# Performance work log

Measured on AMD Instinct MI355X. Metric: run time of the kernel, lower is better.

Reference implementation:

```python
import jax, jax.numpy as jnp
import numpy as np

N = 100000
E = 1600000
IN_DIM, HID, OUT = 512, 128, 16


def setup_inputs() -> dict:
    key = jax.random.key(0)
    ks = jax.random.split(key, 8)
    x = jax.random.normal(ks[0], (N, IN_DIM), dtype=jnp.float32)
    edge_index = jax.random.randint(ks[1], (2, E), 0, N, dtype=jnp.int64)
    # GCNConv params (Glorot-ish scale) and Linear head
    W1 = jax.random.normal(ks[2], (IN_DIM, HID), dtype=jnp.float32) / np.sqrt(IN_DIM)
    b1 = jnp.zeros((HID,), dtype=jnp.float32)
    W2 = jax.random.normal(ks[3], (HID, HID), dtype=jnp.float32) / np.sqrt(HID)
    b2 = jnp.zeros((HID,), dtype=jnp.float32)
    Wl = jax.random.normal(ks[4], (HID, OUT), dtype=jnp.float32) / np.sqrt(HID)
    bl = jnp.zeros((OUT,), dtype=jnp.float32)
    return {"x": x, "edge_index": edge_index, "W1": W1, "b1": b1,
            "W2": W2, "b2": b2, "Wl": Wl, "bl": bl}


def _gcn_conv(x, W, b, src, dst, deg_inv_sqrt, deg_inv):
    # h = x @ W ; out[dst] += norm * h[src]; self-loop adds h[i]/deg[i]
    h = x @ W                                           # [N, D]
    norm = deg_inv_sqrt[src] * deg_inv_sqrt[dst]        # [E]
    msgs = h[src] * norm[:, None]                       # [E, D] gather
    agg = jax.ops.segment_sum(msgs, dst, num_segments=x.shape[0])  # scatter
    agg = agg + h * deg_inv[:, None]                    # self-loop term
    return agg + b


def reference(x, edge_index, W1, b1, W2, b2, Wl, bl):
    src, dst = edge_index[0], edge_index[1]
    n = x.shape[0]
    ones = jnp.ones(src.shape[0], dtype=x.dtype)
    # degree with self-loops (PyG gcn_norm counts in-degree at target + 1)
    deg = jax.ops.segment_sum(ones, dst, num_segments=n) + 1.0
    deg_inv_sqrt = jax.lax.rsqrt(deg)
    deg_inv = 1.0 / deg

    h = _gcn_conv(x, W1, b1, src, dst, deg_inv_sqrt, deg_inv)
    h = jax.nn.relu(h)
    # dropout: inference mode (training=False) -> identity
    h = _gcn_conv(h, W2, b2, src, dst, deg_inv_sqrt, deg_inv)
    embeddings = jax.nn.relu(h)
    out = embeddings @ Wl + bl
    return out, embeddings
```

## Files before the change

kernel.cpp:

```cpp
#include <hip/hip_runtime.h>

#define NN 100000
#define EE 1600000
#define IND 512
#define HIDD 128
#define OUTD 16
#define DEG_BLKS 128
#define GEMM_BLKS 1563

typedef __bf16 bf16x8 __attribute__((ext_vector_type(8)));
typedef float f32x4 __attribute__((ext_vector_type(4)));

__device__ __forceinline__ ushort f2bf(float f) {
    union { float f; uint u; } v; v.f = f;
    uint r = v.u + 0x7FFFu + ((v.u >> 16) & 1u);
    return (ushort)(r >> 16);
}

__global__ void k_prep(const float* __restrict__ W1, const float* __restrict__ W2,
                       ushort* __restrict__ Wt1, ushort* __restrict__ Wt2) {
    int b = blockIdx.x, tid = threadIdx.x;
    if (b < 256) {
        int i = b * 256 + tid;
        int k = i >> 7, n = i & 127;
        Wt1[n * 512 + k] = f2bf(W1[i]);
    } else {
        int i = (b - 256) * 256 + tid;
        int k = i >> 7, n = i & 127;
        Wt2[n * 128 + k] = f2bf(W2[i]);
    }
}

__global__ void k_scan_local(const int* __restrict__ deg, int* __restrict__ incl,
                             int* __restrict__ bsum) {
    __shared__ int s[256];
    int tid = threadIdx.x;
    int i = blockIdx.x * 256 + tid;
    int v = (i < NN) ? deg[i] : 0;
    s[tid] = v;
    __syncthreads();
    for (int off = 1; off < 256; off <<= 1) {
        int t = (tid >= off) ? s[tid - off] : 0;
        __syncthreads();
        s[tid] += t;
        __syncthreads();
    }
    if (i < NN) incl[i] = s[tid];
    if (tid == 255) bsum[blockIdx.x] = s[255];
}

__global__ void k_scan_bsum(const int* __restrict__ bsum, int* __restrict__ boff, int n) {
    __shared__ int s[512];
    int tid = threadIdx.x;
    int v = (tid < n) ? bsum[tid] : 0;
    s[tid] = v;
    __syncthreads();
    for (int off = 1; off < 512; off <<= 1) {
        int t = (tid >= off) ? s[tid - off] : 0;
        __syncthreads();
        s[tid] += t;
        __syncthreads();
    }
    if (tid < n) boff[tid] = s[tid] - v;
}

__global__ void k_scan_final(const int* __restrict__ incl, const int* __restrict__ deg,
                             const int* __restrict__ boff, int* __restrict__ rs,
                             int* __restrict__ cursor, float* __restrict__ dis,
                             float* __restrict__ dinv) {
    int i = blockIdx.x * 256 + threadIdx.x;
    if (i < NN) {
        int d = deg[i];
        int v = incl[i] + boff[i >> 8];
        int start = v - d;
        rs[i] = start;
        cursor[i] = start;
        if (i == NN - 1) rs[NN] = v;
        float df = (float)(d + 1);
        dis[i] = rsqrtf(df);
        dinv[i] = 1.0f / df;
    }
}

__global__ void k_fill(const int* __restrict__ src, const int* __restrict__ dst,
                       const float* __restrict__ dis, int* __restrict__ cursor,
                       int2* __restrict__ ew) {
    int i = blockIdx.x * blockDim.x + threadIdx.x;
    int stride = gridDim.x * blockDim.x;
    for (; i < EE; i += stride) {
        int d = dst[i];
        int s = src[i];
        int pos = atomicAdd(&cursor[d], 1);
        ew[pos] = make_int2(s, __float_as_int(dis[s] * dis[d]));
    }
}

template <int K, bool AFP32>
__device__ __forceinline__ void gemm_body(const void* __restrict__ Ap,
                                          const ushort* __restrict__ Wt,
                                          ushort* __restrict__ C, int M, int blk) {
    __shared__ ushort As[64][40];
    __shared__ ushort Ws[128][40];
    int tid = threadIdx.x;
    int row0 = blk * 64;
    int wid = tid >> 6, lane = tid & 63;
    int wm = (wid & 1) * 32, wn = (wid >> 1) * 64;
    int lm = lane & 15, lk8 = (lane >> 4) * 8;

    f32x4 acc[4][2];
#pragma unroll
    for (int q = 0; q < 4; q++)
#pragma unroll
        for (int r = 0; r < 2; r++) acc[q][r] = (f32x4){0.f, 0.f, 0.f, 0.f};

    int arow = tid >> 2, akg = tid & 3;
    int gr = row0 + arow;

    for (int k0 = 0; k0 < K; k0 += 32) {
        if (AFP32) {
            const float* A = (const float*)Ap;
            float4 v0 = make_float4(0.f, 0.f, 0.f, 0.f), v1 = v0;
            if (gr < M) {
                const float* p = A + (size_t)gr * K + k0 + akg * 8;
                v0 = *(const float4*)(p);
                v1 = *(const float4*)(p + 4);
            }
            uint4 pk;
            pk.x = (uint)f2bf(v0.x) | ((uint)f2bf(v0.y) << 16);
            pk.y = (uint)f2bf(v0.z) | ((uint)f2bf(v0.w) << 16);
            pk.z = (uint)f2bf(v1.x) | ((uint)f2bf(v1.y) << 16);
            pk.w = (uint)f2bf(v1.z) | ((uint)f2bf(v1.w) << 16);
            *(uint4*)&As[arow][akg * 8] = pk;
        } else {
            const ushort* A = (const ushort*)Ap;
            uint4 v = make_uint4(0, 0, 0, 0);
            if (gr < M) v = *(const uint4*)(A + (size_t)gr * K + k0 + akg * 8);
            *(uint4*)&As[arow][akg * 8] = v;
        }
#pragma unroll
        for (int p = 0; p < 2; p++) {
            int idx = p * 256 + tid;
            int n = idx >> 2, kg = idx & 3;
            uint4 v = *(const uint4*)(Wt + (size_t)n * K + k0 + kg * 8);
            *(uint4*)&Ws[n][kg * 8] = v;
        }
        __syncthreads();

        bf16x8 xf[2], wf[4];
#pragma unroll
        for (int r = 0; r < 2; r++) xf[r] = *(const bf16x8*)&As[wm + r * 16 + lm][lk8];
#pragma unroll
        for (int q = 0; q < 4; q++) wf[q] = *(const bf16x8*)&Ws[wn + q * 16 + lm][lk8];
#pragma unroll
        for (int q = 0; q < 4; q++)
#pragma unroll
            for (int r = 0; r < 2; r++)
                acc[q][r] = __builtin_amdgcn_mfma_f32_16x16x32_bf16(wf[q], xf[r], acc[q][r], 0, 0, 0);
        __syncthreads();
    }

    int cn4 = (lane >> 4) * 4;
#pragma unroll
    for (int r = 0; r < 2; r++) {
        int m = row0 + wm + r * 16 + lm;
        if (m < M) {
#pragma unroll
            for (int q = 0; q < 4; q++) {
                int n = wn + q * 16 + cn4;
                uint2 o;
                o.x = (uint)f2bf(acc[q][r][0]) | ((uint)f2bf(acc[q][r][1]) << 16);
                o.y = (uint)f2bf(acc[q][r][2]) | ((uint)f2bf(acc[q][r][3]) << 16);
                *(uint2*)(C + (size_t)m * 128 + n) = o;
            }
        }
    }
}

__global__ __launch_bounds__(256) void k_mega1(const float* __restrict__ x,
                                               const ushort* __restrict__ Wt1,
                                               ushort* __restrict__ C,
                                               const int* __restrict__ dst,
                                               int* __restrict__ deg) {
    if (blockIdx.x < DEG_BLKS) {
        int i = blockIdx.x * 256 + threadIdx.x;
        int stride = DEG_BLKS * 256;
        for (; i < EE; i += stride) atomicAdd(&deg[dst[i]], 1);
    } else {
        gemm_body<IND, true>(x, Wt1, C, NN, blockIdx.x - DEG_BLKS);
    }
}

__global__ __launch_bounds__(256) void k_gemm2(const ushort* __restrict__ A,
                                               const ushort* __restrict__ Wt,
                                               ushort* __restrict__ C) {
    gemm_body<HIDD, false>(A, Wt, C, NN, blockIdx.x);
}

template <bool OUTF32>
__global__ __launch_bounds__(256) void k_agg(const ushort* __restrict__ h,
                                             const int* __restrict__ rs,
                                             const int2* __restrict__ ew,
                                             const float* __restrict__ dinv,
                                             const float* __restrict__ bias,
                                             void* __restrict__ yv) {
    int node = blockIdx.x * 4 + (threadIdx.x >> 6);
    int lane = threadIdx.x & 63;
    if (node >= NN) return;
    int half = lane >> 5, c = lane & 31;
    const uint2* h64 = (const uint2*)h;

    float acc0 = 0.f, acc1 = 0.f, acc2 = 0.f, acc3 = 0.f;
    if (half == 0) {
        float dv = dinv[node];
        uint2 sv = h64[(size_t)node * 32 + c];
        acc0 = __uint_as_float(sv.x << 16) * dv;
        acc1 = __uint_as_float(sv.x & 0xffff0000u) * dv;
        acc2 = __uint_as_float(sv.y << 16) * dv;
        acc3 = __uint_as_float(sv.y & 0xffff0000u) * dv;
    }

    int e = rs[node], e1 = rs[node + 1];

#define EL(i) int2 p##i = ew[e + 2 * i + half]; \
              uint2 g##i = h64[(size_t)(uint)p##i.x * 32 + c];
#define EA(i) { float w##i = __int_as_float(p##i.y); \
    acc0 += w##i * __uint_as_float(g##i.x << 16); \
    acc1 += w##i * __uint_as_float(g##i.x & 0xffff0000u); \
    acc2 += w##i * __uint_as_float(g##i.y << 16); \
    acc3 += w##i * __uint_as_float(g##i.y & 0xffff0000u); }

    for (; e + 16 <= e1; e += 16) {
        EL(0) EL(1) EL(2) EL(3) EL(4) EL(5) EL(6) EL(7)
        EA(0) EA(1) EA(2) EA(3) EA(4) EA(5) EA(6) EA(7)
    }
    for (; e + 4 <= e1; e += 4) {
        EL(0) EL(1)
        EA(0) EA(1)
    }
    if (e + 2 <= e1) {
        EL(0)
        EA(0)
        e += 2;
    }
    if (e < e1 && half == 0) {
        int2 p = ew[e];
        uint2 g = h64[(size_t)(uint)p.x * 32 + c];
        float w = __int_as_float(p.y);
        acc0 += w * __uint_as_float(g.x << 16);
        acc1 += w * __uint_as_float(g.x & 0xffff0000u);
        acc2 += w * __uint_as_float(g.y << 16);
        acc3 += w * __uint_as_float(g.y & 0xffff0000u);
    }
#undef EL
#undef EA

    acc0 += __shfl_xor(acc0, 32, 64);
    acc1 += __shfl_xor(acc1, 32, 64);
    acc2 += __shfl_xor(acc2, 32, 64);
    acc3 += __shfl_xor(acc3, 32, 64);

    if (half == 0) {
        float4 bv = *(const float4*)(bias + c * 4);
        acc0 = fmaxf(acc0 + bv.x, 0.f);
        acc1 = fmaxf(acc1 + bv.y, 0.f);
        acc2 = fmaxf(acc2 + bv.z, 0.f);
        acc3 = fmaxf(acc3 + bv.w, 0.f);
        if (OUTF32) {
            *(float4*)((float*)yv + (size_t)node * 128 + c * 4) =
                make_float4(acc0, acc1, acc2, acc3);
        } else {
            uint2 o;
            o.x = (uint)f2bf(acc0) | ((uint)f2bf(acc1) << 16);
            o.y = (uint)f2bf(acc2) | ((uint)f2bf(acc3) << 16);
            *(uint2*)((ushort*)yv + (size_t)node * 128 + c * 4) = o;
        }
    }
}

__global__ __launch_bounds__(256) void k_out(const float* __restrict__ emb,
                                             const float* __restrict__ Wl,
                                             const float* __restrict__ bl,
                                             float* __restrict__ out) {
    __shared__ float wl_s[128 * 16];
    __shared__ float es[16][129];
    int tid = threadIdx.x;
    int row0 = blockIdx.x * 16;
#pragma unroll
    for (int p = 0; p < 8; p++) wl_s[p * 256 + tid] = Wl[p * 256 + tid];
#pragma unroll
    for (int p = 0; p < 8; p++) {
        int idx = p * 256 + tid;
        int r = idx >> 7, c = idx & 127;
        int gr = row0 + r;
        es[r][c] = (gr < NN) ? emb[(size_t)gr * 128 + c] : 0.0f;
    }
    __syncthreads();
    int r = tid >> 4, o = tid & 15;
    float acc = bl[o];
#pragma unroll
    for (int k = 0; k < 128; k++) acc += es[r][k] * wl_s[k * 16 + o];
    int gr = row0 + r;
    if (gr < NN) out[(size_t)gr * 16 + o] = acc;
}

extern "C" void kernel_launch(void* const* d_in, const int* in_sizes, int n_in,
                              void* d_out, int out_size, void* d_ws, size_t ws_size,
                              hipStream_t stream) {
    const float* x  = (const float*)d_in[0];
    const int* ei   = (const int*)d_in[1];
    const float* W1 = (const float*)d_in[2];
    const float* b1 = (const float*)d_in[3];
    const float* W2 = (const float*)d_in[4];
    const float* b2 = (const float*)d_in[5];
    const float* Wl = (const float*)d_in[6];
    const float* bl = (const float*)d_in[7];
    const int* src = ei;
    const int* dst = ei + EE;

    float* outp = (float*)d_out;
    float* emb  = outp + (size_t)NN * OUTD;

    int2* ew    = (int2*)d_ws;
    ushort* h_a = (ushort*)(ew + EE);
    ushort* h_b = h_a + (size_t)NN * 128;
    ushort* Wt1 = h_b + (size_t)NN * 128;
    ushort* Wt2 = Wt1 + 128 * 512;
    int* deg    = (int*)(Wt2 + 128 * 128);
    float* dis  = (float*)(deg + NN);
    float* dinv = dis + NN;
    int* incl   = (int*)(dinv + NN);
    int* rs     = incl + NN;
    int* cursor = rs + NN + 8;
    int* bsum   = cursor + NN;
    int* boff   = bsum + 512;

    const int NB_N = (NN + 255) / 256;

    hipMemsetAsync(deg, 0, (size_t)NN * sizeof(int), stream);
    k_prep<<<320, 256, 0, stream>>>(W1, W2, Wt1, Wt2);
    k_mega1<<<DEG_BLKS + GEMM_BLKS, 256, 0, stream>>>(x, Wt1, h_a, dst, deg);
    k_scan_local<<<NB_N, 256, 0, stream>>>(deg, incl, bsum);
    k_scan_bsum<<<1, 512, 0, stream>>>(bsum, boff, NB_N);
    k_scan_final<<<NB_N, 256, 0, stream>>>(incl, deg, boff, rs, cursor, dis, dinv);
    k_fill<<<2048, 256, 0, stream>>>(src, dst, dis, cursor, ew);

    k_agg<false><<<(NN + 3) / 4, 256, 0, stream>>>(h_a, rs, ew, dinv, b1, h_b);
    k_gemm2<<<GEMM_BLKS, 256, 0, stream>>>(h_b, Wt2, h_a);
    k_agg<true><<<(NN + 3) / 4, 256, 0, stream>>>(h_a, rs, ew, dinv, b2, emb);
    k_out<<<(NN + 15) / 16, 256, 0, stream>>>(emb, Wl, bl, outp);
}
```

Baseline: 383.0 us.

## Enlarge GEMM tile to 128 rows and prefetch next K-slice into registers

The GEMM block tile grows from 64 to 128 rows, with each warp now covering all 128 output columns, which halves the block count and the number of times the weight slice is reloaded. Global loads for the next K step are issued into registers before the MFMA work on the current step, overlapping memory latency with compute. Out-of-range rows are clamped to the last valid row instead of being zero-filled. In exchange, each thread uses more registers (16 accumulators and the prefetch buffers), which may lower occupancy, and there are now fewer blocks to cover the GPU.

```diff
diff --git a/kernel.cpp b/kernel.cpp
--- a/kernel.cpp
+++ b/kernel.cpp
@@ -6,7 +6,7 @@
 #define HIDD 128
 #define OUTD 16
 #define DEG_BLKS 128
-#define GEMM_BLKS 1563
+#define GEMM_BLKS 782
 
 typedef __bf16 bf16x8 __attribute__((ext_vector_type(8)));
 typedef float f32x4 __attribute__((ext_vector_type(4)));
@@ -99,65 +99,99 @@
 __device__ __forceinline__ void gemm_body(const void* __restrict__ Ap,
                                           const ushort* __restrict__ Wt,
                                           ushort* __restrict__ C, int M, int blk) {
-    __shared__ ushort As[64][40];
+    __shared__ ushort As[128][40];
     __shared__ ushort Ws[128][40];
     int tid = threadIdx.x;
-    int row0 = blk * 64;
+    int row0 = blk * 128;
     int wid = tid >> 6, lane = tid & 63;
-    int wm = (wid & 1) * 32, wn = (wid >> 1) * 64;
+    int wm = wid * 32;
     int lm = lane & 15, lk8 = (lane >> 4) * 8;
 
-    f32x4 acc[4][2];
-#pragma unroll
-    for (int q = 0; q < 4; q++)
+    int srow = tid >> 1;
+    int koff = (tid & 1) * 16;
+    int arow = row0 + srow;
+    if (arow >= M) arow = M - 1;
+    const float* Af = (const float*)Ap;
+    const ushort* Ab = (const ushort*)Ap;
+    const ushort* Wrow = Wt + (size_t)srow * K + koff;
+
+    f32x4 acc[8][2];
+#pragma unroll
+    for (int q = 0; q < 8; q++)
 #pragma unroll
         for (int r = 0; r < 2; r++) acc[q][r] = (f32x4){0.f, 0.f, 0.f, 0.f};
 
-    int arow = tid >> 2, akg = tid & 3;
-    int gr = row0 + arow;
+    float4 a0, a1, a2, a3;
+    uint4 ab0, ab1;
+    uint4 w0, w1;
+
+#define G_LOAD(k0)                                                  \
+    {                                                               \
+        if (AFP32) {                                                \
+            const float* p = Af + (size_t)arow * K + (k0) + koff;   \
+            a0 = *(const float4*)(p);                               \
+            a1 = *(const float4*)(p + 4);                           \
+            a2 = *(const float4*)(p + 8);                           \
+            a3 = *(const float4*)(p + 12);                          \
+        } else {                                                    \
+            const ushort* p = Ab + (size_t)arow * K + (k0) + koff;  \
+            ab0 = *(const uint4*)(p);                               \
+            ab1 = *(const uint4*)(p + 8);                           \
+        }                                                           \
+        const ushort* q_ = Wrow + (k0);                             \
+        w0 = *(const uint4*)(q_);                                   \
+        w1 = *(const uint4*)(q_ + 8);                               \
+    }
+
+#define L_STORE()                                                   \
+    {                                                               \
+        if (AFP32) {                                                \
+            uint4 pk0, pk1;                                         \
+            pk0.x = (uint)f2bf(a0.x) | ((uint)f2bf(a0.y) << 16);    \
+            pk0.y = (uint)f2bf(a0.z) | ((uint)f2bf(a0.w) << 16);    \
+            pk0.z = (uint)f2bf(a1.x) | ((uint)f2bf(a1.y) << 16);    \
+            pk0.w = (uint)f2bf(a1.z) | ((uint)f2bf(a1.w) << 16);    \
+            pk1.x = (uint)f2bf(a2.x) | ((uint)f2bf(a2.y) << 16);    \
+            pk1.y = (uint)f2bf(a2.z) | ((uint)f2bf(a2.w) << 16);    \
+            pk1.z = (uint)f2bf(a3.x) | ((uint)f2bf(a3.y) << 16);    \
+            pk1.w = (uint)f2bf(a3.z) | ((uint)f2bf(a3.w) << 16);    \
+            *(uint4*)&As[srow][koff] = pk0;                         \
+            *(uint4*)&As[srow][koff + 8] = pk1;                     \
+        } else {                                                    \
+            *(uint4*)&As[srow][koff] = ab0;                         \
+            *(uint4*)&As[srow][koff + 8] = ab1;                     \
+        }                                                           \
+        *(uint4*)&Ws[srow][koff] = w0;                              \
+        *(uint4*)&Ws[srow][koff + 8] = w1;                          \
+    }
+
+    G_LOAD(0)
+    L_STORE()
+    __syncthreads();
 
     for (int k0 = 0; k0 < K; k0 += 32) {
-        if (AFP32) {
-            const float* A = (const float*)Ap;
-            float4 v0 = make_float4(0.f, 0.f, 0.f, 0.f), v1 = v0;
-            if (gr < M) {
-                const float* p = A + (size_t)gr * K + k0 + akg * 8;
-                v0 = *(const float4*)(p);
-                v1 = *(const float4*)(p + 4);
-            }
-            uint4 pk;
-            pk.x = (uint)f2bf(v0.x) | ((uint)f2bf(v0.y) << 16);
-            pk.y = (uint)f2bf(v0.z) | ((uint)f2bf(v0.w) << 16);
-            pk.z = (uint)f2bf(v1.x) | ((uint)f2bf(v1.y) << 16);
-            pk.w = (uint)f2bf(v1.z) | ((uint)f2bf(v1.w) << 16);
-            *(uint4*)&As[arow][akg * 8] = pk;
-        } else {
-            const ushort* A = (const ushort*)Ap;
-            uint4 v = make_uint4(0, 0, 0, 0);
-            if (gr < M) v = *(const uint4*)(A + (size_t)gr * K + k0 + akg * 8);
-            *(uint4*)&As[arow][akg * 8] = v;
-        }
-#pragma unroll
-        for (int p = 0; p < 2; p++) {
-            int idx = p * 256 + tid;
-            int n = idx >> 2, kg = idx & 3;
-            uint4 v = *(const uint4*)(Wt + (size_t)n * K + k0 + kg * 8);
-            *(uint4*)&Ws[n][kg * 8] = v;
-        }
-        __syncthreads();
-
-        bf16x8 xf[2], wf[4];
+        bool notlast = (k0 + 32 < K);
+        if (notlast) G_LOAD(k0 + 32)
+
+        bf16x8 xf[2], wf[8];
 #pragma unroll
         for (int r = 0; r < 2; r++) xf[r] = *(const bf16x8*)&As[wm + r * 16 + lm][lk8];
 #pragma unroll
-        for (int q = 0; q < 4; q++) wf[q] = *(const bf16x8*)&Ws[wn + q * 16 + lm][lk8];
-#pragma unroll
-        for (int q = 0; q < 4; q++)
+        for (int q = 0; q < 8; q++) wf[q] = *(const bf16x8*)&Ws[q * 16 + lm][lk8];
+#pragma unroll
+        for (int q = 0; q < 8; q++)
 #pragma unroll
             for (int r = 0; r < 2; r++)
                 acc[q][r] = __builtin_amdgcn_mfma_f32_16x16x32_bf16(wf[q], xf[r], acc[q][r], 0, 0, 0);
-        __syncthreads();
-    }
+
+        if (notlast) {
+            __syncthreads();
+            L_STORE()
+            __syncthreads();
+        }
+    }
+#undef G_LOAD
+#undef L_STORE
 
     int cn4 = (lane >> 4) * 4;
 #pragma unroll
@@ -165,8 +199,8 @@
         int m = row0 + wm + r * 16 + lm;
         if (m < M) {
 #pragma unroll
-            for (int q = 0; q < 4; q++) {
-                int n = wn + q * 16 + cn4;
+            for (int q = 0; q < 8; q++) {
+                int n = q * 16 + cn4;
                 uint2 o;
                 o.x = (uint)f2bf(acc[q][r][0]) | ((uint)f2bf(acc[q][r][1]) << 16);
                 o.y = (uint)f2bf(acc[q][r][2]) | ((uint)f2bf(acc[q][r][3]) << 16);
```

After: 389.5 us. No clear change (+1.7%).

## Double-buffer GEMM with direct global-to-LDS loads and 128-row tiles

Applied to the files above, without the earlier changes.

The GEMM body now uses 128x128 block tiles with each wave covering 32 rows across all 128 columns. It double-buffers A and W in LDS, filling them with global_load_lds DMA, XOR-swizzled to avoid bank conflicts. Manual vmcnt waits let the next k-tile load overlap the current MFMA work. For fp32 input, conversion to bf16 moves from staging into the fragment read, which doubles the A LDS footprint and adds register pressure from 16 accumulators per wave.

```diff
diff --git a/kernel.cpp b/kernel.cpp
--- a/kernel.cpp
+++ b/kernel.cpp
@@ -6,7 +6,7 @@
 #define HIDD 128
 #define OUTD 16
 #define DEG_BLKS 128
-#define GEMM_BLKS 1563
+#define GEMM_BLKS 782
 
 typedef __bf16 bf16x8 __attribute__((ext_vector_type(8)));
 typedef float f32x4 __attribute__((ext_vector_type(4)));
@@ -16,6 +16,17 @@
     uint r = v.u + 0x7FFFu + ((v.u >> 16) & 1u);
     return (ushort)(r >> 16);
 }
+
+__device__ __forceinline__ uint pk2bf(float a, float b) {
+    __bf16 x = (__bf16)a, y = (__bf16)b;
+    ushort ux = *(ushort*)&x, uy = *(ushort*)&y;
+    return (uint)ux | ((uint)uy << 16);
+}
+
+#define GLDS16(src, dst)                                              \
+    __builtin_amdgcn_global_load_lds(                                 \
+        (const __attribute__((address_space(1))) void*)(src),         \
+        (__attribute__((address_space(3))) void*)(dst), 16, 0, 0)
 
 __global__ void k_prep(const float* __restrict__ W1, const float* __restrict__ W2,
                        ushort* __restrict__ Wt1, ushort* __restrict__ Wt2) {
@@ -99,64 +110,112 @@
 __device__ __forceinline__ void gemm_body(const void* __restrict__ Ap,
                                           const ushort* __restrict__ Wt,
                                           ushort* __restrict__ C, int M, int blk) {
-    __shared__ ushort As[64][40];
-    __shared__ ushort Ws[128][40];
+    constexpr int NT = K / 32;
+    constexpr int ABYTES = AFP32 ? 128 * 32 * 4 : 128 * 32 * 2;
+    constexpr int WBYTES = 128 * 32 * 2;
+    __shared__ char smem[2 * (ABYTES + WBYTES)];
+
     int tid = threadIdx.x;
-    int row0 = blk * 64;
+    int row0 = blk * 128;
     int wid = tid >> 6, lane = tid & 63;
-    int wm = (wid & 1) * 32, wn = (wid >> 1) * 64;
+    int wm = wid * 32;
     int lm = lane & 15, lk8 = (lane >> 4) * 8;
 
-    f32x4 acc[4][2];
-#pragma unroll
-    for (int q = 0; q < 4; q++)
+    const float* Af = (const float*)Ap;
+    const ushort* Ab16 = (const ushort*)Ap;
+
+    f32x4 acc[8][2];
+#pragma unroll
+    for (int q = 0; q < 8; q++)
 #pragma unroll
         for (int r = 0; r < 2; r++) acc[q][r] = (f32x4){0.f, 0.f, 0.f, 0.f};
 
-    int arow = tid >> 2, akg = tid & 3;
-    int gr = row0 + arow;
-
-    for (int k0 = 0; k0 < K; k0 += 32) {
+    auto stage = [&](int bi, int k0) {
+        char* Abase = smem + bi * ABYTES;
+        char* Wbase = smem + 2 * ABYTES + bi * WBYTES;
         if (AFP32) {
-            const float* A = (const float*)Ap;
-            float4 v0 = make_float4(0.f, 0.f, 0.f, 0.f), v1 = v0;
-            if (gr < M) {
-                const float* p = A + (size_t)gr * K + k0 + akg * 8;
-                v0 = *(const float4*)(p);
-                v1 = *(const float4*)(p + 4);
+#pragma unroll
+            for (int j = 0; j < 4; j++) {
+                int c = wid * 4 + j;
+                int rp = c * 8 + (lane >> 3);
+                int sl = (lane & 7) ^ (rp & 7);
+                int gr2 = row0 + rp; if (gr2 >= M) gr2 = M - 1;
+                GLDS16(Af + (size_t)gr2 * K + k0 + sl * 4, Abase + c * 1024);
             }
-            uint4 pk;
-            pk.x = (uint)f2bf(v0.x) | ((uint)f2bf(v0.y) << 16);
-            pk.y = (uint)f2bf(v0.z) | ((uint)f2bf(v0.w) << 16);
-            pk.z = (uint)f2bf(v1.x) | ((uint)f2bf(v1.y) << 16);
-            pk.w = (uint)f2bf(v1.z) | ((uint)f2bf(v1.w) << 16);
-            *(uint4*)&As[arow][akg * 8] = pk;
         } else {
-            const ushort* A = (const ushort*)Ap;
-            uint4 v = make_uint4(0, 0, 0, 0);
-            if (gr < M) v = *(const uint4*)(A + (size_t)gr * K + k0 + akg * 8);
-            *(uint4*)&As[arow][akg * 8] = v;
-        }
-#pragma unroll
-        for (int p = 0; p < 2; p++) {
-            int idx = p * 256 + tid;
-            int n = idx >> 2, kg = idx & 3;
-            uint4 v = *(const uint4*)(Wt + (size_t)n * K + k0 + kg * 8);
-            *(uint4*)&Ws[n][kg * 8] = v;
-        }
-        __syncthreads();
-
-        bf16x8 xf[2], wf[4];
-#pragma unroll
-        for (int r = 0; r < 2; r++) xf[r] = *(const bf16x8*)&As[wm + r * 16 + lm][lk8];
-#pragma unroll
-        for (int q = 0; q < 4; q++) wf[q] = *(const bf16x8*)&Ws[wn + q * 16 + lm][lk8];
-#pragma unroll
-        for (int q = 0; q < 4; q++)
+#pragma unroll
+            for (int j = 0; j < 2; j++) {
+                int c = wid * 2 + j;
+                int rp = c * 16 + (lane >> 2);
+                int sl = (lane & 3) ^ (rp & 3);
+                int gr2 = row0 + rp; if (gr2 >= M) gr2 = M - 1;
+                GLDS16(Ab16 + (size_t)gr2 * K + k0 + sl * 8, Abase + c * 1024);
+            }
+        }
+#pragma unroll
+        for (int j = 0; j < 2; j++) {
+            int c = wid * 2 + j;
+            int rp = c * 16 + (lane >> 2);
+            int sl = (lane & 3) ^ (rp & 3);
+            GLDS16(Wt + (size_t)rp * K + k0 + sl * 8, Wbase + c * 1024);
+        }
+    };
+
+    stage(0, 0);
+
+    int cur = 0;
+    for (int t = 0; t < NT; t++) {
+        if (t + 1 < NT) {
+            stage((t + 1) & 1, (t + 1) * 32);
+            if (AFP32) asm volatile("s_waitcnt vmcnt(6)" ::: "memory");
+            else       asm volatile("s_waitcnt vmcnt(4)" ::: "memory");
+        } else {
+            asm volatile("s_waitcnt vmcnt(0)" ::: "memory");
+        }
+        __builtin_amdgcn_s_barrier();
+
+        char* Abase = smem + cur * ABYTES;
+        char* Wbase = smem + 2 * ABYTES + cur * WBYTES;
+        bf16x8 xf[2], wf[8];
+        if (AFP32) {
+#pragma unroll
+            for (int r = 0; r < 2; r++) {
+                int r_ = wm + r * 16 + lm;
+                int s0 = lk8 >> 2;
+                f32x4 a0 = *(const f32x4*)(Abase + r_ * 128 + (((s0)     ^ (r_ & 7)) << 4));
+                f32x4 a1 = *(const f32x4*)(Abase + r_ * 128 + (((s0 + 1) ^ (r_ & 7)) << 4));
+                uint4 u;
+                u.x = pk2bf(a0[0], a0[1]);
+                u.y = pk2bf(a0[2], a0[3]);
+                u.z = pk2bf(a1[0], a1[1]);
+                u.w = pk2bf(a1[2], a1[3]);
+                xf[r] = *(bf16x8*)&u;
+            }
+        } else {
+#pragma unroll
+            for (int r = 0; r < 2; r++) {
+                int r_ = wm + r * 16 + lm;
+                int s = lk8 >> 3;
+                uint4 u = *(const uint4*)(Abase + r_ * 64 + ((s ^ (r_ & 3)) << 4));
+                xf[r] = *(bf16x8*)&u;
+            }
+        }
+#pragma unroll
+        for (int q = 0; q < 8; q++) {
+            int n_ = q * 16 + lm;
+            int s = lk8 >> 3;
+            uint4 u = *(const uint4*)(Wbase + n_ * 64 + ((s ^ (n_ & 3)) << 4));
+            wf[q] = *(bf16x8*)&u;
+        }
+#pragma unroll
+        for (int q = 0; q < 8; q++)
 #pragma unroll
             for (int r = 0; r < 2; r++)
                 acc[q][r] = __builtin_amdgcn_mfma_f32_16x16x32_bf16(wf[q], xf[r], acc[q][r], 0, 0, 0);
-        __syncthreads();
+
+        asm volatile("" ::: "memory");
+        __builtin_amdgcn_s_barrier();
+        cur ^= 1;
     }
 
     int cn4 = (lane >> 4) * 4;
@@ -165,8 +224,8 @@
         int m = row0 + wm + r * 16 + lm;
         if (m < M) {
 #pragma unroll
-            for (int q = 0; q < 4; q++) {
-                int n = wn + q * 16 + cn4;
+            for (int q = 0; q < 8; q++) {
+                int n = q * 16 + cn4;
                 uint2 o;
                 o.x = (uint)f2bf(acc[q][r][0]) | ((uint)f2bf(acc[q][r][1]) << 16);
                 o.y = (uint)f2bf(acc[q][r][2]) | ((uint)f2bf(acc[q][r][3]) << 16);
```

After: 376.8 us. Within noise of the previous version (-1.6%).

## Rewrite GEMM to load fragments directly from global with register double-buffering

Applied to the files above, without the earlier changes.

The GEMM body no longer stages A and W tiles through shared memory with two barriers per k-step. Each wave now loads its MFMA fragments straight from global memory into registers and alternates two register sets so the next k-slice loads while the current one multiplies. Rows per block double from 64 to 128, and each wave covers all 128 output columns, which halves the GEMM block count. This removes LDS traffic and barriers but makes every wave reload the full weight matrix from global/L2 and raises register pressure, which may reduce occupancy.

```diff
diff --git a/kernel.cpp b/kernel.cpp
--- a/kernel.cpp
+++ b/kernel.cpp
@@ -6,7 +6,7 @@
 #define HIDD 128
 #define OUTD 16
 #define DEG_BLKS 128
-#define GEMM_BLKS 1563
+#define GEMM_BLKS 782
 
 typedef __bf16 bf16x8 __attribute__((ext_vector_type(8)));
 typedef float f32x4 __attribute__((ext_vector_type(4)));
@@ -15,6 +15,12 @@
     union { float f; uint u; } v; v.f = f;
     uint r = v.u + 0x7FFFu + ((v.u >> 16) & 1u);
     return (ushort)(r >> 16);
+}
+
+__device__ __forceinline__ uint pk2bf(float a, float b) {
+    __bf16 x = (__bf16)a, y = (__bf16)b;
+    ushort ux = *(ushort*)&x, uy = *(ushort*)&y;
+    return (uint)ux | ((uint)uy << 16);
 }
 
 __global__ void k_prep(const float* __restrict__ W1, const float* __restrict__ W2,
@@ -99,65 +105,89 @@
 __device__ __forceinline__ void gemm_body(const void* __restrict__ Ap,
                                           const ushort* __restrict__ Wt,
                                           ushort* __restrict__ C, int M, int blk) {
-    __shared__ ushort As[64][40];
-    __shared__ ushort Ws[128][40];
+    constexpr int NT = K / 32;
     int tid = threadIdx.x;
-    int row0 = blk * 64;
+    int row0 = blk * 128;
     int wid = tid >> 6, lane = tid & 63;
-    int wm = (wid & 1) * 32, wn = (wid >> 1) * 64;
+    int wm = wid * 32;
     int lm = lane & 15, lk8 = (lane >> 4) * 8;
 
-    f32x4 acc[4][2];
-#pragma unroll
-    for (int q = 0; q < 4; q++)
+    int ra = row0 + wm + lm;
+    int rb = ra + 16;
+    if (ra >= M) ra = M - 1;
+    if (rb >= M) rb = M - 1;
+
+    const float* Af = (const float*)Ap;
+    const ushort* Ab = (const ushort*)Ap;
+    const ushort* Wl0 = Wt + (size_t)lm * K + lk8;
+
+    f32x4 acc[8][2];
+#pragma unroll
+    for (int q = 0; q < 8; q++)
 #pragma unroll
         for (int r = 0; r < 2; r++) acc[q][r] = (f32x4){0.f, 0.f, 0.f, 0.f};
 
-    int arow = tid >> 2, akg = tid & 3;
-    int gr = row0 + arow;
-
-    for (int k0 = 0; k0 < K; k0 += 32) {
-        if (AFP32) {
-            const float* A = (const float*)Ap;
-            float4 v0 = make_float4(0.f, 0.f, 0.f, 0.f), v1 = v0;
-            if (gr < M) {
-                const float* p = A + (size_t)gr * K + k0 + akg * 8;
-                v0 = *(const float4*)(p);
-                v1 = *(const float4*)(p + 4);
-            }
-            uint4 pk;
-            pk.x = (uint)f2bf(v0.x) | ((uint)f2bf(v0.y) << 16);
-            pk.y = (uint)f2bf(v0.z) | ((uint)f2bf(v0.w) << 16);
-            pk.z = (uint)f2bf(v1.x) | ((uint)f2bf(v1.y) << 16);
-            pk.w = (uint)f2bf(v1.z) | ((uint)f2bf(v1.w) << 16);
-            *(uint4*)&As[arow][akg * 8] = pk;
-        } else {
-            const ushort* A = (const ushort*)Ap;
-            uint4 v = make_uint4(0, 0, 0, 0);
-            if (gr < M) v = *(const uint4*)(A + (size_t)gr * K + k0 + akg * 8);
-            *(uint4*)&As[arow][akg * 8] = v;
-        }
-#pragma unroll
-        for (int p = 0; p < 2; p++) {
-            int idx = p * 256 + tid;
-            int n = idx >> 2, kg = idx & 3;
-            uint4 v = *(const uint4*)(Wt + (size_t)n * K + k0 + kg * 8);
-            *(uint4*)&Ws[n][kg * 8] = v;
-        }
-        __syncthreads();
-
-        bf16x8 xf[2], wf[4];
-#pragma unroll
-        for (int r = 0; r < 2; r++) xf[r] = *(const bf16x8*)&As[wm + r * 16 + lm][lk8];
-#pragma unroll
-        for (int q = 0; q < 4; q++) wf[q] = *(const bf16x8*)&Ws[wn + q * 16 + lm][lk8];
-#pragma unroll
-        for (int q = 0; q < 4; q++)
-#pragma unroll
-            for (int r = 0; r < 2; r++)
-                acc[q][r] = __builtin_amdgcn_mfma_f32_16x16x32_bf16(wf[q], xf[r], acc[q][r], 0, 0, 0);
-        __syncthreads();
-    }
+    bf16x8 wA[8], wB[8];
+    float4 sA0, sA1, sA2, sA3;
+    float4 sB0, sB1, sB2, sB3;
+    bf16x8 xA0, xA1, xB0, xB1;
+
+#define LW(buf, k0)                                                        \
+    {                                                                      \
+        _Pragma("unroll") for (int q = 0; q < 8; q++)                      \
+            buf[q] = *(const bf16x8*)(Wl0 + (size_t)q * 16 * K + (k0));    \
+    }
+#define LA32(s0, s1, s2, s3, k0)                                           \
+    {                                                                      \
+        const float* pa = Af + (size_t)ra * K + (k0) + lk8;                \
+        const float* pb = Af + (size_t)rb * K + (k0) + lk8;                \
+        s0 = *(const float4*)pa; s1 = *(const float4*)(pa + 4);            \
+        s2 = *(const float4*)pb; s3 = *(const float4*)(pb + 4);            \
+    }
+#define CVTA(s0, s1, s2, s3, x0, x1)                                       \
+    {                                                                      \
+        uint4 u, v;                                                        \
+        u.x = pk2bf(s0.x, s0.y); u.y = pk2bf(s0.z, s0.w);                  \
+        u.z = pk2bf(s1.x, s1.y); u.w = pk2bf(s1.z, s1.w);                  \
+        v.x = pk2bf(s2.x, s2.y); v.y = pk2bf(s2.z, s2.w);                  \
+        v.z = pk2bf(s3.x, s3.y); v.w = pk2bf(s3.z, s3.w);                  \
+        x0 = *(bf16x8*)&u; x1 = *(bf16x8*)&v;                              \
+    }
+#define LA16(x0, x1, k0)                                                   \
+    {                                                                      \
+        x0 = *(const bf16x8*)(Ab + (size_t)ra * K + (k0) + lk8);           \
+        x1 = *(const bf16x8*)(Ab + (size_t)rb * K + (k0) + lk8);           \
+    }
+#define MM(wf, x0, x1)                                                     \
+    {                                                                      \
+        _Pragma("unroll") for (int q = 0; q < 8; q++) {                    \
+            acc[q][0] = __builtin_amdgcn_mfma_f32_16x16x32_bf16(           \
+                wf[q], x0, acc[q][0], 0, 0, 0);                            \
+            acc[q][1] = __builtin_amdgcn_mfma_f32_16x16x32_bf16(           \
+                wf[q], x1, acc[q][1], 0, 0, 0);                            \
+        }                                                                  \
+    }
+
+    if (AFP32) { LA32(sA0, sA1, sA2, sA3, 0) } else { LA16(xA0, xA1, 0) }
+    LW(wA, 0)
+
+    for (int t = 0; t < NT; t += 2) {
+        int k1 = (t + 1) * 32;
+        int k2 = ((t + 2) & (NT - 1)) * 32;
+        if (AFP32) { LA32(sB0, sB1, sB2, sB3, k1) } else { LA16(xB0, xB1, k1) }
+        LW(wB, k1)
+        if (AFP32) CVTA(sA0, sA1, sA2, sA3, xA0, xA1)
+        MM(wA, xA0, xA1)
+        if (AFP32) { LA32(sA0, sA1, sA2, sA3, k2) } else { LA16(xA0, xA1, k2) }
+        LW(wA, k2)
+        if (AFP32) CVTA(sB0, sB1, sB2, sB3, xB0, xB1)
+        MM(wB, xB0, xB1)
+    }
+#undef LW
+#undef LA32
+#undef CVTA
+#undef LA16
+#undef MM
 
     int cn4 = (lane >> 4) * 4;
 #pragma unroll
@@ -165,8 +195,8 @@
         int m = row0 + wm + r * 16 + lm;
         if (m < M) {
 #pragma unroll
-            for (int q = 0; q < 4; q++) {
-                int n = wn + q * 16 + cn4;
+            for (int q = 0; q < 8; q++) {
+                int n = q * 16 + cn4;
                 uint2 o;
                 o.x = (uint)f2bf(acc[q][r][0]) | ((uint)f2bf(acc[q][r][1]) << 16);
                 o.y = (uint)f2bf(acc[q][r][2]) | ((uint)f2bf(acc[q][r][3]) << 16);
```

Result: slower. 436.3 us (+13.9%).
